# Optimization experiments

Hardware: AMD Instinct MI355X
Metric: run time of the kernel (lower is better)

## Reference

```python
import jax, jax.numpy as jnp
import numpy as np

N = 50000      # num nodes (== num segments for aggregation)
E = 800000     # num edges
D_IN = 128
D_OUT = 128


def setup_inputs() -> dict:
    key = jax.random.key(0)
    k1, k2, k3, k4, k5, k6 = jax.random.split(key, 6)
    x = jax.random.normal(k1, (N, D_IN), dtype=jnp.float32)
    edge_rows = jax.random.randint(k2, (E,), 0, N, dtype=jnp.int32)
    edge_cols = jax.random.randint(k3, (E,), 0, N, dtype=jnp.int32)
    edge_vals = jax.random.uniform(k4, (E,), dtype=jnp.float32)
    stdv = 1.0 / np.sqrt(D_OUT)
    weight = jax.random.uniform(k5, (D_IN, D_OUT), dtype=jnp.float32, minval=-stdv, maxval=stdv)
    root_weight = jax.random.uniform(k6, (D_IN, D_OUT), dtype=jnp.float32, minval=-stdv, maxval=stdv)
    return {"x": x, "edge_rows": edge_rows, "edge_cols": edge_cols,
            "edge_vals": edge_vals, "weight": weight, "root_weight": root_weight}


def reference(x, edge_rows, edge_cols, edge_vals, weight, root_weight):
    # support = x @ W                                  [N, D_OUT]
    support = jnp.dot(x, weight)
    # out = spmm(adj, support): adj in COO form.
    # message per edge: adj[r, c] * support[c]         [E, D_OUT]
    msgs = support[edge_cols] * edge_vals[:, None]
    agg = jax.ops.segment_sum(msgs, edge_rows, num_segments=N)  # [N, D_OUT]
    # out += x @ W_root  (bias=False configuration)
    return agg + jnp.dot(x, root_weight)
```

## Files before the change

### kernel.cpp

```cpp
#include <hip/hip_runtime.h>

#define D 128
#define NCK 512
#define RPB 32
#define BCAP 1024
#define SCANW 2048
#define RAWB 17408

typedef short short8 __attribute__((ext_vector_type(8)));
typedef float v4f __attribute__((ext_vector_type(4)));
typedef float float2v __attribute__((ext_vector_type(2)));

static __device__ __forceinline__ unsigned short f2bf(float f) {
    unsigned u = __builtin_bit_cast(unsigned, f);
    u = (u + 0x7FFFu + ((u >> 16) & 1u)) >> 16;
    return (unsigned short)u;
}

__global__ __launch_bounds__(256) void wt_prep(
    const float* __restrict__ W, const float* __restrict__ Wr,
    unsigned short* __restrict__ Wt)
{
    const int gid = (int)blockIdx.x * 256 + (int)threadIdx.x;
    const int k  = gid >> 8;
    const int nn = gid & 255;
    const float v = (nn < D) ? W[k * D + nn] : Wr[k * D + (nn - D)];
    Wt[nn * D + k] = f2bf(v);
}

__global__ __launch_bounds__(256) void prep_gemm(
    const int* __restrict__ rows, const int* __restrict__ cols,
    const float* __restrict__ vals,
    unsigned* __restrict__ pkT, int2* __restrict__ sortedB,
    const float* __restrict__ x, const unsigned short* __restrict__ Wt,
    unsigned short* __restrict__ support, unsigned short* __restrict__ rootbuf,
    int M, int E, int nbuck, int chunk)
{
    __shared__ __align__(16) char raw[RAWB];
    __shared__ int wsumK[4];
    const int t = threadIdx.x;
    const int lane = t & 63, w = t >> 6;

    if ((int)blockIdx.x < NCK) {
        int* hist = (int*)raw;
        int* cur  = hist + SCANW;
        const int c = blockIdx.x;

        #pragma unroll
        for (int j = 0; j < SCANW / 256; ++j) hist[t + j * 256] = 0;
        __syncthreads();

        const int base = c * chunk;
        const int endv = min(base + chunk, E);
        for (int e = base + t; e < endv; e += 256)
            atomicAdd(&hist[rows[e] >> 5], 1);
        __syncthreads();

        int lv[8];
        int ssum = 0;
        #pragma unroll
        for (int j = 0; j < 8; ++j) { lv[j] = hist[8 * t + j]; ssum += lv[j]; }
        int s = ssum;
        #pragma unroll
        for (int d = 1; d < 64; d <<= 1) {
            const int u = __shfl_up(s, d);
            if (lane >= d) s += u;
        }
        if (lane == 63) wsumK[w] = s;
        __syncthreads();
        int woff = 0;
        #pragma unroll
        for (int j = 0; j < 4; ++j) if (j < w) woff += wsumK[j];
        int run = woff + s - ssum;
        #pragma unroll
        for (int j = 0; j < 8; ++j) {
            const int idx = 8 * t + j;
            cur[idx] = run;
            if (idx < nbuck)
                pkT[(size_t)c * nbuck + idx] =
                    ((unsigned)lv[j] << 16) | (unsigned)run;
            run += lv[j];
        }
        __syncthreads();

        for (int e = base + t; e < endv; e += 256) {
            const int r  = rows[e];
            const int cc = cols[e];
            const float v = vals[e];
            const int pos = atomicAdd(&cur[r >> 5], 1);
            sortedB[(size_t)base + pos] =
                make_int2(((r & (RPB - 1)) << 16) | cc, __float_as_int(v));
        }
        return;
    }

    unsigned short (*As)[136] = (unsigned short (*)[136])raw;
    const int nl = lane & 15, quad = lane >> 4;
    const int rowBase = ((int)blockIdx.x - NCK) * 64;

    {
        const int r = t & 63;
        const int seg = t >> 6;
        const int row = rowBase + r;
        unsigned short tmp[32];
        if (row < M) {
            const float4* src = (const float4*)(x + (size_t)row * D + seg * 32);
            #pragma unroll
            for (int j = 0; j < 8; ++j) {
                const float4 v = src[j];
                tmp[j * 4 + 0] = f2bf(v.x); tmp[j * 4 + 1] = f2bf(v.y);
                tmp[j * 4 + 2] = f2bf(v.z); tmp[j * 4 + 3] = f2bf(v.w);
            }
        } else {
            #pragma unroll
            for (int j = 0; j < 32; ++j) tmp[j] = 0;
        }
        #pragma unroll
        for (int j = 0; j < 4; ++j)
            *(short8*)&As[r][seg * 32 + j * 8] = *(const short8*)&tmp[j * 8];
    }

    short8 bfrag[4][4];
    {
        const unsigned short* wbase = Wt + (size_t)(w * 64 + nl) * D + quad * 8;
        #pragma unroll
        for (int nt = 0; nt < 4; ++nt)
            #pragma unroll
            for (int c = 0; c < 4; ++c)
                bfrag[c][nt] = *(const short8*)(wbase + (size_t)nt * 16 * D + c * 32);
    }
    __syncthreads();

    v4f acc[4][4] = {};
    #pragma unroll
    for (int c = 0; c < 4; ++c) {
        short8 afr[4];
        #pragma unroll
        for (int mt = 0; mt < 4; ++mt)
            afr[mt] = *(const short8*)&As[mt * 16 + nl][c * 32 + quad * 8];
        #pragma unroll
        for (int mt = 0; mt < 4; ++mt)
            #pragma unroll
            for (int nt = 0; nt < 4; ++nt)
                acc[mt][nt] = __builtin_amdgcn_mfma_f32_16x16x32_bf16(
                    afr[mt], bfrag[c][nt], acc[mt][nt], 0, 0, 0);
    }

    const int cbase = (w & 1) * 64;
    unsigned short* dst = (w < 2) ? support : rootbuf;
    #pragma unroll
    for (int mt = 0; mt < 4; ++mt)
        #pragma unroll
        for (int reg = 0; reg < 4; ++reg) {
            const int row = rowBase + mt * 16 + quad * 4 + reg;
            if (row < M) {
                #pragma unroll
                for (int nt = 0; nt < 4; ++nt)
                    dst[(size_t)row * D + cbase + nt * 16 + nl] = f2bf(acc[mt][nt][reg]);
            }
        }
}

__global__ __launch_bounds__(256) void transpose_pk(
    const unsigned* __restrict__ pkT, unsigned* __restrict__ pkTt, int nbuck)
{
    __shared__ unsigned tile[64][65];
    const int cb = (int)blockIdx.x & 7;
    const int bb = (int)blockIdx.x >> 3;
    const int t = threadIdx.x;
    for (int i = t; i < 64 * 64; i += 256) {
        const int lc = i & 63, lr = i >> 6;
        const int b = bb * 64 + lc, c = cb * 64 + lr;
        tile[lr][lc] = (b < nbuck) ? pkT[(size_t)c * nbuck + b] : 0u;
    }
    __syncthreads();
    for (int i = t; i < 64 * 64; i += 256) {
        const int lc = i & 63, lr = i >> 6;
        const int b = bb * 64 + lr, c = cb * 64 + lc;
        if (b < nbuck) pkTt[(size_t)b * NCK + c] = tile[lc][lr];
    }
}

__global__ __launch_bounds__(256) void sort_aggregate(
    const unsigned* __restrict__ pkTt, const int2* __restrict__ sortedB,
    const unsigned short* __restrict__ support,
    const unsigned short* __restrict__ rootbuf,
    float* __restrict__ out, int M, int nbuck, int chunk)
{
    __shared__ int2 stage[BCAP];
    __shared__ unsigned rowList[BCAP];
    __shared__ int wsum[4];
    __shared__ int rh[RPB];
    __shared__ int rs[RPB + 1];
    __shared__ int rcur[RPB];
    const int b = blockIdx.x, t = threadIdx.x;
    const int lane = t & 63, w = t >> 6;

    const uint2 pk2 = *(const uint2*)(pkTt + (size_t)b * NCK + 2 * t);
    const int cnt0 = (int)(pk2.x >> 16), off0 = (int)(pk2.x & 0xFFFFu);
    const int cnt1 = (int)(pk2.y >> 16), off1 = (int)(pk2.y & 0xFFFFu);
    int s = cnt0 + cnt1;
    #pragma unroll
    for (int d = 1; d < 64; d <<= 1) {
        const int u = __shfl_up(s, d);
        if (lane >= d) s += u;
    }
    if (lane == 63) wsum[w] = s;
    __syncthreads();
    int woff = 0, tot = 0;
    #pragma unroll
    for (int j = 0; j < 4; ++j) { const int v = wsum[j]; if (j < w) woff += v; tot += v; }
    const int incl = woff + s;
    const int base1 = incl - cnt1;
    const int base0 = base1 - cnt0;
    {
        const int2* src = sortedB + (size_t)(2 * t) * chunk + off0;
        int lim = min(base0 + cnt0, BCAP) - base0; if (lim < 0) lim = 0;
        for (int k = 0; k < lim; ++k) stage[base0 + k] = src[k];
    }
    {
        const int2* src = sortedB + (size_t)(2 * t + 1) * chunk + off1;
        int lim = min(base1 + cnt1, BCAP) - base1; if (lim < 0) lim = 0;
        for (int k = 0; k < lim; ++k) stage[base1 + k] = src[k];
    }
    if (t < RPB) rh[t] = 0;
    __syncthreads();

    const int T = min(tot, BCAP);
    for (int e = t; e < T; e += 256) atomicAdd(&rh[stage[e].x >> 16], 1);
    __syncthreads();
    if (t < 64) {
        const int mine = (t < RPB) ? rh[t] : 0;
        int v = mine;
        #pragma unroll
        for (int d = 1; d < RPB; d <<= 1) {
            const int u = __shfl_up(v, d);
            if (lane >= d) v += u;
        }
        if (t < RPB) {
            rs[t] = v - mine; rcur[t] = v - mine;
            if (t == RPB - 1) rs[RPB] = v;
        }
    }
    __syncthreads();
    for (int e = t; e < T; e += 256) {
        const int2 ed = stage[e];
        const int rib = ed.x >> 16;
        const int pos = atomicAdd(&rcur[rib], 1);
        rowList[pos] = ((unsigned)f2bf(__int_as_float(ed.y)) << 16)
                     | (unsigned)(ed.x & 0xFFFF);
    }
    __syncthreads();

    for (int r = w; r < RPB; r += 4) {
        const int row = b * RPB + r;
        if (row >= M) continue;
        const int st = rs[r], e2 = rs[r + 1];
        float ax = 0.f, ay = 0.f;
        int i = st;

        for (; i + 16 <= e2; i += 16) {
            unsigned d[16];
            #pragma unroll
            for (int j = 0; j < 16; ++j) d[j] = rowList[i + j];
            unsigned p[16];
            #pragma unroll
            for (int j = 0; j < 16; ++j)
                p[j] = *(const unsigned*)(support + (size_t)(d[j] & 0xFFFF) * D + lane * 2);
            #pragma unroll
            for (int j = 0; j < 16; ++j) {
                const float v = __builtin_bit_cast(float, d[j] & 0xFFFF0000u);
                ax += __builtin_bit_cast(float, p[j] << 16) * v;
                ay += __builtin_bit_cast(float, p[j] & 0xFFFF0000u) * v;
            }
        }
        if (i + 8 <= e2) {
            unsigned d[8];
            #pragma unroll
            for (int j = 0; j < 8; ++j) d[j] = rowList[i + j];
            unsigned p[8];
            #pragma unroll
            for (int j = 0; j < 8; ++j)
                p[j] = *(const unsigned*)(support + (size_t)(d[j] & 0xFFFF) * D + lane * 2);
            #pragma unroll
            for (int j = 0; j < 8; ++j) {
                const float v = __builtin_bit_cast(float, d[j] & 0xFFFF0000u);
                ax += __builtin_bit_cast(float, p[j] << 16) * v;
                ay += __builtin_bit_cast(float, p[j] & 0xFFFF0000u) * v;
            }
            i += 8;
        }
        if (i < e2) {
            const int m = e2 - i;
            unsigned d[8];
            #pragma unroll
            for (int j = 0; j < 8; ++j) {
                const int idx = i + (j < m ? j : m - 1);
                const unsigned q = rowList[idx];
                d[j] = (j < m) ? q : (q & 0xFFFFu);
            }
            unsigned p[8];
            #pragma unroll
            for (int j = 0; j < 8; ++j)
                p[j] = *(const unsigned*)(support + (size_t)(d[j] & 0xFFFF) * D + lane * 2);
            #pragma unroll
            for (int j = 0; j < 8; ++j) {
                const float v = __builtin_bit_cast(float, d[j] & 0xFFFF0000u);
                ax += __builtin_bit_cast(float, p[j] << 16) * v;
                ay += __builtin_bit_cast(float, p[j] & 0xFFFF0000u) * v;
            }
        }

        const unsigned pr = *(const unsigned*)(rootbuf + (size_t)row * D + lane * 2);
        float2v ov;
        ov.x = ax + __builtin_bit_cast(float, pr << 16);
        ov.y = ay + __builtin_bit_cast(float, pr & 0xFFFF0000u);
        __builtin_nontemporal_store(ov, (float2v*)(out + (size_t)row * D + lane * 2));
    }
}

extern "C" void kernel_launch(void* const* d_in, const int* in_sizes, int n_in,
                              void* d_out, int out_size, void* d_ws, size_t ws_size,
                              hipStream_t stream) {
    const float* x     = (const float*)d_in[0];
    const int*   erows = (const int*)d_in[1];
    const int*   ecols = (const int*)d_in[2];
    const float* evals = (const float*)d_in[3];
    const float* W     = (const float*)d_in[4];
    const float* Wr    = (const float*)d_in[5];
    float* out = (float*)d_out;

    const int M = in_sizes[0] / D;
    const int E = in_sizes[1];

    const int nbuck = (M + RPB - 1) / RPB;
    const int chunk = (E + NCK - 1) / NCK;
    const int nGemm = (M + 63) / 64;

    unsigned short* support = (unsigned short*)d_ws;
    unsigned short* rootbuf = support + (size_t)M * D;
    unsigned short* Wt      = rootbuf + (size_t)M * D;
    unsigned* pkT   = (unsigned*)(Wt + 2 * D * D);
    unsigned* pkTt  = pkT + (size_t)NCK * nbuck;
    int2*  sortedB  = (int2*)(pkTt + (size_t)nbuck * NCK);

    const int nTb = (nbuck + 63) / 64;

    wt_prep<<<128, 256, 0, stream>>>(W, Wr, Wt);
    prep_gemm<<<NCK + nGemm, 256, 0, stream>>>(
        erows, ecols, evals, pkT, sortedB, x, Wt, support, rootbuf,
        M, E, nbuck, chunk);
    transpose_pk<<<8 * nTb, 256, 0, stream>>>(pkT, pkTt, nbuck);
    sort_aggregate<<<nbuck, 256, 0, stream>>>(pkTt, sortedB,
                                              support, rootbuf, out, M, nbuck, chunk);
}
```

Before: 154.2 us.

## Halve edge chunks and write bucket table transposed, dropping transpose kernel

Cuts the number of edge-partition chunks from 512 to 256 so each chunk holds twice as many edges. The histogram kernel now writes its count/offset table straight into bucket-major layout, and a swizzled chunk index spreads those scattered writes. This removes the separate transpose kernel and its launch. The aggregation kernel reads one chunk entry per thread instead of two. Larger chunks mean longer serial atomic scatter loops per block, and the scattered column writes may coalesce poorly.

```diff
diff --git a/kernel.cpp b/kernel.cpp
--- a/kernel.cpp
+++ b/kernel.cpp
@@ -1,7 +1,7 @@
 #include <hip/hip_runtime.h>
 
 #define D 128
-#define NCK 512
+#define NCK 256
 #define RPB 32
 #define BCAP 1024
 #define SCANW 2048
@@ -31,7 +31,7 @@
 __global__ __launch_bounds__(256) void prep_gemm(
     const int* __restrict__ rows, const int* __restrict__ cols,
     const float* __restrict__ vals,
-    unsigned* __restrict__ pkT, int2* __restrict__ sortedB,
+    unsigned* __restrict__ pkTt, int2* __restrict__ sortedB,
     const float* __restrict__ x, const unsigned short* __restrict__ Wt,
     unsigned short* __restrict__ support, unsigned short* __restrict__ rootbuf,
     int M, int E, int nbuck, int chunk)
@@ -44,7 +44,7 @@
     if ((int)blockIdx.x < NCK) {
         int* hist = (int*)raw;
         int* cur  = hist + SCANW;
-        const int c = blockIdx.x;
+        const int c = (((int)blockIdx.x & 7) << 5) + ((int)blockIdx.x >> 3);
 
         #pragma unroll
         for (int j = 0; j < SCANW / 256; ++j) hist[t + j * 256] = 0;
@@ -77,7 +77,7 @@
             const int idx = 8 * t + j;
             cur[idx] = run;
             if (idx < nbuck)
-                pkT[(size_t)c * nbuck + idx] =
+                pkTt[(size_t)idx * NCK + c] =
                     ((unsigned)lv[j] << 16) | (unsigned)run;
             run += lv[j];
         }
@@ -159,26 +159,6 @@
                     dst[(size_t)row * D + cbase + nt * 16 + nl] = f2bf(acc[mt][nt][reg]);
             }
         }
-}
-
-__global__ __launch_bounds__(256) void transpose_pk(
-    const unsigned* __restrict__ pkT, unsigned* __restrict__ pkTt, int nbuck)
-{
-    __shared__ unsigned tile[64][65];
-    const int cb = (int)blockIdx.x & 7;
-    const int bb = (int)blockIdx.x >> 3;
-    const int t = threadIdx.x;
-    for (int i = t; i < 64 * 64; i += 256) {
-        const int lc = i & 63, lr = i >> 6;
-        const int b = bb * 64 + lc, c = cb * 64 + lr;
-        tile[lr][lc] = (b < nbuck) ? pkT[(size_t)c * nbuck + b] : 0u;
-    }
-    __syncthreads();
-    for (int i = t; i < 64 * 64; i += 256) {
-        const int lc = i & 63, lr = i >> 6;
-        const int b = bb * 64 + lr, c = cb * 64 + lc;
-        if (b < nbuck) pkTt[(size_t)b * NCK + c] = tile[lc][lr];
-    }
 }
 
 __global__ __launch_bounds__(256) void sort_aggregate(
@@ -196,10 +176,9 @@
     const int b = blockIdx.x, t = threadIdx.x;
     const int lane = t & 63, w = t >> 6;
 
-    const uint2 pk2 = *(const uint2*)(pkTt + (size_t)b * NCK + 2 * t);
-    const int cnt0 = (int)(pk2.x >> 16), off0 = (int)(pk2.x & 0xFFFFu);
-    const int cnt1 = (int)(pk2.y >> 16), off1 = (int)(pk2.y & 0xFFFFu);
-    int s = cnt0 + cnt1;
+    const unsigned pk = pkTt[(size_t)b * NCK + t];
+    const int cnt = (int)(pk >> 16), off = (int)(pk & 0xFFFFu);
+    int s = cnt;
     #pragma unroll
     for (int d = 1; d < 64; d <<= 1) {
         const int u = __shfl_up(s, d);
@@ -210,18 +189,11 @@
     int woff = 0, tot = 0;
     #pragma unroll
     for (int j = 0; j < 4; ++j) { const int v = wsum[j]; if (j < w) woff += v; tot += v; }
-    const int incl = woff + s;
-    const int base1 = incl - cnt1;
-    const int base0 = base1 - cnt0;
+    const int base0 = woff + s - cnt;
     {
-        const int2* src = sortedB + (size_t)(2 * t) * chunk + off0;
-        int lim = min(base0 + cnt0, BCAP) - base0; if (lim < 0) lim = 0;
+        const int2* src = sortedB + (size_t)t * chunk + off;
+        int lim = min(base0 + cnt, BCAP) - base0; if (lim < 0) lim = 0;
         for (int k = 0; k < lim; ++k) stage[base0 + k] = src[k];
-    }
-    {
-        const int2* src = sortedB + (size_t)(2 * t + 1) * chunk + off1;
-        int lim = min(base1 + cnt1, BCAP) - base1; if (lim < 0) lim = 0;
-        for (int k = 0; k < lim; ++k) stage[base1 + k] = src[k];
     }
     if (t < RPB) rh[t] = 0;
     __syncthreads();
@@ -340,17 +312,13 @@
     unsigned short* support = (unsigned short*)d_ws;
     unsigned short* rootbuf = support + (size_t)M * D;
     unsigned short* Wt      = rootbuf + (size_t)M * D;
-    unsigned* pkT   = (unsigned*)(Wt + 2 * D * D);
-    unsigned* pkTt  = pkT + (size_t)NCK * nbuck;
+    unsigned* pkTt  = (unsigned*)(Wt + 2 * D * D);
     int2*  sortedB  = (int2*)(pkTt + (size_t)nbuck * NCK);
-
-    const int nTb = (nbuck + 63) / 64;
 
     wt_prep<<<128, 256, 0, stream>>>(W, Wr, Wt);
     prep_gemm<<<NCK + nGemm, 256, 0, stream>>>(
-        erows, ecols, evals, pkT, sortedB, x, Wt, support, rootbuf,
+        erows, ecols, evals, pkTt, sortedB, x, Wt, support, rootbuf,
         M, E, nbuck, chunk);
-    transpose_pk<<<8 * nTb, 256, 0, stream>>>(pkT, pkTt, nbuck);
     sort_aggregate<<<nbuck, 256, 0, stream>>>(pkTt, sortedB,
                                               support, rootbuf, out, M, nbuck, chunk);
 }
```

New measurement: 148.4 us. -3.8%, faster.
